# Kernel tuning notes

Measured on AMD Instinct MI355X. Metric: run time of the kernel, lower is better.

Reference implementation:

```python
import jax, jax.numpy as jnp
import numpy as np

B, S, D = 4, 1024, 1024
H = 16
DK = D // H  # per-head dim_q = dim_k = 64
DFF = 4096
EPS = 1e-5


def _layer_norm(x, g, b):
    m = jnp.mean(x, axis=-1, keepdims=True)
    v = jnp.mean((x - m) ** 2, axis=-1, keepdims=True)
    return (x - m) / jnp.sqrt(v + EPS) * g + b


def setup_inputs() -> dict:
    key = jax.random.key(0)
    ks = jax.random.split(key, 16)
    sd = 1.0 / np.sqrt(D)
    sk = 1.0 / np.sqrt(H * DK)
    sf = 1.0 / np.sqrt(DFF)
    return {
        "src": jax.random.normal(ks[0], (B, S, D), jnp.float32),
        # stacked per-head projections (torch loops over H separate nn.Linear)
        "Wq": jax.random.uniform(ks[1], (H, D, DK), jnp.float32, -sd, sd),
        "bq": jax.random.uniform(ks[2], (H, DK), jnp.float32, -sd, sd),
        "Wk": jax.random.uniform(ks[3], (H, D, DK), jnp.float32, -sd, sd),
        "bk": jax.random.uniform(ks[4], (H, DK), jnp.float32, -sd, sd),
        "Wv": jax.random.uniform(ks[5], (H, D, DK), jnp.float32, -sd, sd),
        "bv": jax.random.uniform(ks[6], (H, DK), jnp.float32, -sd, sd),
        "Wo": jax.random.uniform(ks[7], (H * DK, D), jnp.float32, -sk, sk),
        "bo": jax.random.uniform(ks[8], (D,), jnp.float32, -sk, sk),
        "g1": jnp.ones((D,), jnp.float32),
        "be1": jnp.zeros((D,), jnp.float32),
        "W1": jax.random.uniform(ks[9], (D, DFF), jnp.float32, -sd, sd),
        "b1": jax.random.uniform(ks[10], (DFF,), jnp.float32, -sd, sd),
        "W2": jax.random.uniform(ks[11], (DFF, D), jnp.float32, -sf, sf),
        "b2": jax.random.uniform(ks[12], (D,), jnp.float32, -sf, sf),
        "g2": jnp.ones((D,), jnp.float32),
        "be2": jnp.zeros((D,), jnp.float32),
    }


def reference(src, Wq, bq, Wk, bk, Wv, bv, Wo, bo, g1, be1, W1, b1, W2, b2, g2, be2):
    # multi-head attention (all heads batched via einsum instead of python loop)
    q = jnp.einsum("bsd,hdk->bhsk", src, Wq) + bq[None, :, None, :]
    k = jnp.einsum("bsd,hdk->bhsk", src, Wk) + bk[None, :, None, :]
    v = jnp.einsum("bsd,hdk->bhsk", src, Wv) + bv[None, :, None, :]
    scale = jnp.asarray(DK, src.dtype) ** 0.5  # query.size(-1) ** 0.5
    scores = jnp.einsum("bhsk,bhtk->bhst", q, k) / scale
    attn = jax.nn.softmax(scores, axis=-1)
    o = jnp.einsum("bhst,bhtk->bhsk", attn, v)  # [B,H,S,DK]
    o = o.transpose(0, 2, 1, 3).reshape(src.shape[0], src.shape[1], H * DK)
    attn_out = o @ Wo + bo
    x = _layer_norm(src + attn_out, g1, be1)
    ffn = jax.nn.relu(x @ W1 + b1) @ W2 + b2
    return _layer_norm(x + ffn, g2, be2)
```

## Files before the change

### kernel.cpp

```cpp
#include <hip/hip_runtime.h>
#include <hip/hip_bf16.h>

#define DEV __device__ __forceinline__

typedef __attribute__((ext_vector_type(8))) short bf16x8;
typedef __attribute__((ext_vector_type(4))) float f32x4;
typedef __attribute__((ext_vector_type(4))) short short4v;
typedef __attribute__((ext_vector_type(2))) unsigned uint2v;

DEV short f2bf(float f) {
    union { float f; unsigned u; } x; x.f = f;
    unsigned u = x.u;
    unsigned r = (u + 0x7fffu + ((u >> 16) & 1u)) >> 16;
    return (short)r;
}

DEV float bf2f(short s) {
    union { unsigned u; float f; } x;
    x.u = ((unsigned)(unsigned short)s) << 16;
    return x.f;
}

DEV unsigned cvtpk(float a, float b) {
    unsigned r;
    asm("v_cvt_pk_bf16_f32 %0, %1, %2" : "=v"(r) : "v"(a), "v"(b));
    return r;
}

#define GLD16(g, l)                                                         \
    __builtin_amdgcn_global_load_lds(                                       \
        (const __attribute__((address_space(1))) void*)(g),                 \
        (__attribute__((address_space(3))) void*)(l), 16, 0, 0)

#define WAITV(n) asm volatile("s_waitcnt vmcnt(" #n ")" ::: "memory")
#define SBAR()   asm volatile("s_barrier" ::: "memory")
#define LGKM0()                                              \
    asm volatile("s_waitcnt lgkmcnt(0)" ::: "memory");       \
    __builtin_amdgcn_sched_barrier(0)


__global__ __launch_bounds__(256) void k_cast(const float* __restrict__ in,
                                              short* __restrict__ out, int n4) {
    int i = blockIdx.x * 256 + threadIdx.x;
    if (i >= n4) return;
    float4 v = ((const float4*)in)[i];
    short4v o;
    o[0] = f2bf(v.x); o[1] = f2bf(v.y); o[2] = f2bf(v.z); o[3] = f2bf(v.w);
    ((short4v*)out)[i] = o;
}

__global__ __launch_bounds__(256) void k_tr(const float* __restrict__ in,
                                            short* __restrict__ out,
                                            int R, int C,
                                            long in_hs, long out_hs) {
    in  += (size_t)blockIdx.z * in_hs;
    out += (size_t)blockIdx.z * out_hs;
    __shared__ short tile[64][68];
    const int t = threadIdx.x;
    const int r0 = blockIdx.y * 64, c0 = blockIdx.x * 64;
    const int lr = t >> 4, lc4 = (t & 15) * 4;
#pragma unroll
    for (int it = 0; it < 4; ++it) {
        int r = lr + it * 16;
        float4 v = *(const float4*)(in + (size_t)(r0 + r) * C + c0 + lc4);
        tile[lc4 + 0][r] = f2bf(v.x);
        tile[lc4 + 1][r] = f2bf(v.y);
        tile[lc4 + 2][r] = f2bf(v.z);
        tile[lc4 + 3][r] = f2bf(v.w);
    }
    __syncthreads();
#pragma unroll
    for (int it = 0; it < 4; ++it) {
        int c = lr + it * 16;
        short4v o;
        o[0] = tile[c][lc4 + 0];
        o[1] = tile[c][lc4 + 1];
        o[2] = tile[c][lc4 + 2];
        o[3] = tile[c][lc4 + 3];
        *(short4v*)(out + (size_t)(c0 + c) * R + r0 + lc4) = o;
    }
}

template <int MODE>
__global__ __launch_bounds__(512, 2) void k_gemm8(
    const short* __restrict__ A, const short* __restrict__ BT,
    int K, int NT,
    const float* __restrict__ f0, const float* __restrict__ f1,
    const float* __restrict__ f2,
    void* __restrict__ o0, void* __restrict__ o1, void* __restrict__ o2) {
    __shared__ short lds[2][2][2][128 * 64];
    const int t = threadIdx.x;
    const int w = t >> 6, l = t & 63;
    const int l16 = l & 15, lg = l >> 4;
    const int wm = w >> 2, wn = w & 3;
    const int bn = blockIdx.x, bm = blockIdx.y;
    const int koff = blockIdx.z * NT * 64;
    const short* Ab = A + (size_t)bm * 256 * K + koff;
    const short* Bb = BT + (size_t)bn * 256 * K + koff;
    const int srow = l >> 3;
    const int scol = ((l & 7) ^ srow) * 8;
    const int offk0 = ((0 + lg) ^ (l16 & 7)) * 8;
    const int offk1 = ((4 + lg) ^ (l16 & 7)) * 8;

    f32x4 acc[8][4] = {};

    auto stg = [&](int buf, int op, int h, int kt) {
#pragma unroll
        for (int i = 0; i < 2; ++i) {
            int row = h * 128 + w * 16 + i * 8 + srow;
            GLD16((op ? Bb : Ab) + (size_t)row * K + (size_t)kt * 64 + scol,
                  &lds[buf][op][h][(w * 16 + i * 8) * 64]);
        }
    };

    stg(0, 0, 0, 0); stg(0, 0, 1, 0);
    stg(0, 1, 0, 0); stg(0, 1, 1, 0);
    const int t1p = (NT > 1) ? 1 : 0;
    stg(1, 1, 0, t1p); stg(1, 1, 1, t1p);
    WAITV(4);
    SBAR();

    for (int kt = 0; kt < NT; ++kt) {
        const int cur = kt & 1, nxt = cur ^ 1;
        const int t1 = (kt + 1 < NT) ? kt + 1 : NT - 1;
        const int t2 = (kt + 2 < NT) ? kt + 2 : NT - 1;
        bf16x8 a0[4][2], a1[4][2], b0[2][2], b1[2][2];

#pragma unroll
        for (int m = 0; m < 4; ++m) {
            a0[m][0] = *(const bf16x8*)&lds[cur][0][wm][(m * 16 + l16) * 64 + offk0];
            a0[m][1] = *(const bf16x8*)&lds[cur][0][wm][(m * 16 + l16) * 64 + offk1];
        }
#pragma unroll
        for (int n = 0; n < 2; ++n) {
            int r = (wn & 1) * 64 + n * 16 + l16;
            b0[n][0] = *(const bf16x8*)&lds[cur][1][wn >> 1][r * 64 + offk0];
            b0[n][1] = *(const bf16x8*)&lds[cur][1][wn >> 1][r * 64 + offk1];
        }
        stg(nxt, 0, 0, t1);
        SBAR();
        LGKM0();
        __builtin_amdgcn_s_setprio(1);
#pragma unroll
        for (int m = 0; m < 4; ++m)
#pragma unroll
            for (int n = 0; n < 2; ++n) {
                acc[m][n] = __builtin_amdgcn_mfma_f32_16x16x32_bf16(a0[m][0], b0[n][0], acc[m][n], 0, 0, 0);
                acc[m][n] = __builtin_amdgcn_mfma_f32_16x16x32_bf16(a0[m][1], b0[n][1], acc[m][n], 0, 0, 0);
            }
        __builtin_amdgcn_s_setprio(0);
        SBAR();

#pragma unroll
        for (int n = 0; n < 2; ++n) {
            int r = (wn & 1) * 64 + (n + 2) * 16 + l16;
            b1[n][0] = *(const bf16x8*)&lds[cur][1][wn >> 1][r * 64 + offk0];
            b1[n][1] = *(const bf16x8*)&lds[cur][1][wn >> 1][r * 64 + offk1];
        }
        stg(nxt, 0, 1, t1);
        SBAR();
        LGKM0();
        __builtin_amdgcn_s_setprio(1);
#pragma unroll
        for (int m = 0; m < 4; ++m)
#pragma unroll
            for (int n = 0; n < 2; ++n) {
                acc[m][n + 2] = __builtin_amdgcn_mfma_f32_16x16x32_bf16(a0[m][0], b1[n][0], acc[m][n + 2], 0, 0, 0);
                acc[m][n + 2] = __builtin_amdgcn_mfma_f32_16x16x32_bf16(a0[m][1], b1[n][1], acc[m][n + 2], 0, 0, 0);
            }
        __builtin_amdgcn_s_setprio(0);
        SBAR();

#pragma unroll
        for (int m = 0; m < 4; ++m) {
            a1[m][0] = *(const bf16x8*)&lds[cur][0][wm][((m + 4) * 16 + l16) * 64 + offk0];
            a1[m][1] = *(const bf16x8*)&lds[cur][0][wm][((m + 4) * 16 + l16) * 64 + offk1];
        }
        stg(cur, 1, 0, t2);
        SBAR();
        LGKM0();
        __builtin_amdgcn_s_setprio(1);
#pragma unroll
        for (int m = 0; m < 4; ++m)
#pragma unroll
            for (int n = 0; n < 2; ++n) {
                acc[m + 4][n + 2] = __builtin_amdgcn_mfma_f32_16x16x32_bf16(a1[m][0], b1[n][0], acc[m + 4][n + 2], 0, 0, 0);
                acc[m + 4][n + 2] = __builtin_amdgcn_mfma_f32_16x16x32_bf16(a1[m][1], b1[n][1], acc[m + 4][n + 2], 0, 0, 0);
            }
        __builtin_amdgcn_s_setprio(0);
        SBAR();

        stg(cur, 1, 1, t2);
        SBAR();
        __builtin_amdgcn_s_setprio(1);
#pragma unroll
        for (int m = 0; m < 4; ++m)
#pragma unroll
            for (int n = 0; n < 2; ++n) {
                acc[m + 4][n] = __builtin_amdgcn_mfma_f32_16x16x32_bf16(a1[m][0], b0[n][0], acc[m + 4][n], 0, 0, 0);
                acc[m + 4][n] = __builtin_amdgcn_mfma_f32_16x16x32_bf16(a1[m][1], b0[n][1], acc[m + 4][n], 0, 0, 0);
            }
        __builtin_amdgcn_s_setprio(0);
        WAITV(4);
        SBAR();
    }
    WAITV(0);

    const int N = gridDim.x * 256;
#pragma unroll
    for (int m = 0; m < 8; ++m) {
        int rowbase = bm * 256 + wm * 128 + m * 16 + lg * 4;
#pragma unroll
        for (int n = 0; n < 4; ++n) {
            int col = bn * 256 + wn * 64 + n * 16 + l16;
            if constexpr (MODE == 0) {
                int p = col >> 10, c1 = col & 1023;
                int hh = c1 >> 6, dk = c1 & 63;
                const float* bias = (p == 0) ? f0 : (p == 1) ? f1 : f2;
                float bvl = bias[c1];
                float qs = (p == 0) ? 0.18033688011112042f : 1.0f;
                int b = rowbase >> 10, s = rowbase & 1023;
                if (p == 2) {
                    short4v vv;
#pragma unroll
                    for (int rr = 0; rr < 4; ++rr) vv[rr] = f2bf(acc[m][n][rr] + bvl);
                    *(short4v*)((short*)o2 + (((size_t)(b * 16 + hh) * 64 + dk) << 10) + s) = vv;
                } else {
                    short* dst = (p == 0) ? (short*)o0 : (short*)o1;
#pragma unroll
                    for (int rr = 0; rr < 4; ++rr)
                        dst[(((size_t)(b * 16 + hh) << 10) + s + rr) * 64 + dk] =
                            f2bf((acc[m][n][rr] + bvl) * qs);
                }
            } else if constexpr (MODE == 2) {
                float bvl = f0[col];
#pragma unroll
                for (int rr = 0; rr < 4; ++rr) {
                    size_t idx = (size_t)(rowbase + rr) * N + col;
                    float y = acc[m][n][rr] + bvl;
                    ((short*)o0)[idx] = f2bf(y > 0.f ? y : 0.f);
                }
            } else {
                const int Mtot = gridDim.y * 256;
                short* dst = (blockIdx.z < 3)
                    ? (short*)o0 + (size_t)blockIdx.z * Mtot * N
                    : (short*)o1;
                size_t base = (size_t)rowbase * N + col;
#pragma unroll
                for (int rr = 0; rr < 4; ++rr)
                    dst[base + (size_t)rr * N] = f2bf(acc[m][n][rr]);
            }
        }
    }
}

__global__ __launch_bounds__(512, 4) void k_attn(const short* __restrict__ Q,
                                                 const short* __restrict__ Kt,
                                                 const short* __restrict__ VT,
                                                 short* __restrict__ O) {
    __shared__ short Kl[2][64 * 64];
    __shared__ short Vl[2][64 * 64];
    __shared__ short Pl[8][16 * 64];
    const int bh = blockIdx.x;
    const int qb = blockIdx.y;
    const int t = threadIdx.x;
    const int w = t >> 6, l = t & 63;
    const int l16 = l & 15, lg = l >> 4;
    const int sw = l16 & 7;
    const int pmask = (l16 & 7) << 1;
    const int srow = l >> 3;
    const int scol = ((l & 7) ^ srow) * 8;

    const short* Qb = Q + ((size_t)bh * 1024 + qb * 128 + w * 16 + l16) * 64 + lg * 8;
    bf16x8 qf0 = *(const bf16x8*)Qb;
    bf16x8 qf1 = *(const bf16x8*)(Qb + 32);

    const short* Kbase = Kt + (size_t)bh * (1024 * 64);
    const short* Vbase = VT + (size_t)bh * (64 * 1024);

    const float THR = 11.5415603f;

    bf16x8 ones;
#pragma unroll
    for (int i = 0; i < 8; ++i) ones[i] = (short)0x3F80;

    float m = -1e30f;
    f32x4 oacc[4] = {};
    f32x4 oaccS = {};

    auto stage = [&](int buf, int t0) {
        int roww = w * 8;
        GLD16(Kbase + (size_t)(t0 + roww + srow) * 64 + scol,
              &Kl[buf][roww * 64]);
        GLD16(Vbase + (size_t)(roww + srow) * 1024 + t0 + scol,
              &Vl[buf][roww * 64]);
    };

    auto compute = [&](int cur) {
        f32x4 s[4];
#pragma unroll
        for (int n = 0; n < 4; ++n) {
            bf16x8 kf0 = *(const bf16x8*)&Kl[cur][(n * 16 + l16) * 64 + (lg ^ sw) * 8];
            bf16x8 kf1 = *(const bf16x8*)&Kl[cur][(n * 16 + l16) * 64 + ((4 + lg) ^ sw) * 8];
            f32x4 a = {0.f, 0.f, 0.f, 0.f};
            a = __builtin_amdgcn_mfma_f32_16x16x32_bf16(kf0, qf0, a, 0, 0, 0);
            a = __builtin_amdgcn_mfma_f32_16x16x32_bf16(kf1, qf1, a, 0, 0, 0);
            s[n] = a;
        }
        float m1 = fmaxf(fmaxf(s[0][0], s[0][1]), s[0][2]);
        float m2 = fmaxf(fmaxf(s[0][3], s[1][0]), s[1][1]);
        float m3 = fmaxf(fmaxf(s[1][2], s[1][3]), s[2][0]);
        float m4 = fmaxf(fmaxf(s[2][1], s[2][2]), s[2][3]);
        float m5 = fmaxf(fmaxf(s[3][0], s[3][1]), s[3][2]);
        float mx = fmaxf(fmaxf(m1, m2), m3);
        mx = fmaxf(fmaxf(m4, m5), fmaxf(mx, s[3][3]));
        mx = fmaxf(mx, __shfl_xor(mx, 16));
        mx = fmaxf(mx, __shfl_xor(mx, 32));

        if (__any(mx > m + THR)) {
            float mn = fmaxf(m, mx);
            float al = exp2f(m - mn);
            m = mn;
#pragma unroll
            for (int n = 0; n < 4; ++n)
#pragma unroll
                for (int r = 0; r < 4; ++r) s[n][r] = exp2f(s[n][r] - m);
#pragma unroll
            for (int r = 0; r < 4; ++r) {
                float alr = __shfl(al, lg * 4 + r);
                oaccS[r] *= alr;
#pragma unroll
                for (int n = 0; n < 4; ++n) oacc[n][r] *= alr;
            }
        } else {
#pragma unroll
            for (int n = 0; n < 4; ++n)
#pragma unroll
                for (int r = 0; r < 4; ++r) s[n][r] = exp2f(s[n][r] - m);
        }
#pragma unroll
        for (int n = 0; n < 4; ++n) {
            uint2v pv;
            pv[0] = cvtpk(s[n][0], s[n][1]);
            pv[1] = cvtpk(s[n][2], s[n][3]);
            int g = (n * 4 + lg) ^ pmask;
            *(uint2v*)((char*)Pl[w] + l16 * 128 + g * 8) = pv;
        }
#pragma unroll
        for (int kk = 0; kk < 2; ++kk) {
            int gp = (8 * kk + 2 * lg) ^ pmask;
            bf16x8 pa = *(const bf16x8*)((const char*)Pl[w] + l16 * 128 + gp * 8);
            oaccS = __builtin_amdgcn_mfma_f32_16x16x32_bf16(pa, ones, oaccS, 0, 0, 0);
#pragma unroll
            for (int n = 0; n < 4; ++n) {
                bf16x8 vb = *(const bf16x8*)&Vl[cur][(n * 16 + l16) * 64 +
                                                     ((kk * 4 + lg) ^ sw) * 8];
                oacc[n] = __builtin_amdgcn_mfma_f32_16x16x32_bf16(pa, vb, oacc[n],
                                                                  0, 0, 0);
            }
        }
    };

    stage(0, 0);
    for (int ti = 0; ti < 15; ++ti) {
        int cur = ti & 1;
        stage(cur ^ 1, (ti + 1) * 64);
        WAITV(2);
        SBAR();
        compute(cur);
        SBAR();
    }
    WAITV(0);
    SBAR();
    compute(1);

    const int b = bh >> 4, h = bh & 15;
#pragma unroll
    for (int r = 0; r < 4; ++r) {
        float inv = 1.f / oaccS[r];
        size_t row = (size_t)(b * 1024 + qb * 128 + w * 16 + lg * 4 + r);
#pragma unroll
        for (int n = 0; n < 4; ++n)
            O[row * 1024 + h * 64 + n * 16 + l16] = f2bf(oacc[n][r] * inv);
    }
}

__global__ __launch_bounds__(256) void k_lnwo(const short* __restrict__ p012,
                                              const short* __restrict__ p3,
                                              const float* __restrict__ bias,
                                              const float* __restrict__ resid,
                                              const float* __restrict__ g,
                                              const float* __restrict__ be,
                                              float* __restrict__ of,
                                              short* __restrict__ ob) {
    const int row = blockIdx.x, t = threadIdx.x;
    float4 x = ((const float4*)(resid + ((size_t)row << 10)))[t];
    float4 bv = ((const float4*)bias)[t];
    x.x += bv.x; x.y += bv.y; x.z += bv.z; x.w += bv.w;
#pragma unroll
    for (int kz = 0; kz < 3; ++kz) {
        short4v p = ((const short4v*)(p012 + (((size_t)kz * 4096 + row) << 10)))[t];
        x.x += bf2f(p[0]); x.y += bf2f(p[1]); x.z += bf2f(p[2]); x.w += bf2f(p[3]);
    }
    {
        short4v p = ((const short4v*)(p3 + ((size_t)row << 10)))[t];
        x.x += bf2f(p[0]); x.y += bf2f(p[1]); x.z += bf2f(p[2]); x.w += bf2f(p[3]);
    }
    float s = x.x + x.y + x.z + x.w;
    float s2 = x.x * x.x + x.y * x.y + x.z * x.z + x.w * x.w;
#pragma unroll
    for (int mm = 1; mm < 64; mm <<= 1) {
        s += __shfl_xor(s, mm);
        s2 += __shfl_xor(s2, mm);
    }
    __shared__ float red[8];
    if ((t & 63) == 0) { red[t >> 6] = s; red[4 + (t >> 6)] = s2; }
    __syncthreads();
    s = red[0] + red[1] + red[2] + red[3];
    s2 = red[4] + red[5] + red[6] + red[7];
    float mean = s * (1.f / 1024.f);
    float var = s2 * (1.f / 1024.f) - mean * mean;
    float rstd = rsqrtf(var + 1e-5f);
    int c = t * 4;
    float4 y;
    y.x = (x.x - mean) * rstd * g[c + 0] + be[c + 0];
    y.y = (x.y - mean) * rstd * g[c + 1] + be[c + 1];
    y.z = (x.z - mean) * rstd * g[c + 2] + be[c + 2];
    y.w = (x.w - mean) * rstd * g[c + 3] + be[c + 3];
    ((float4*)(of + ((size_t)row << 10)))[t] = y;
    short4v o;
    o[0] = f2bf(y.x); o[1] = f2bf(y.y); o[2] = f2bf(y.z); o[3] = f2bf(y.w);
    ((short4v*)(ob + ((size_t)row << 10)))[t] = o;
}

__global__ __launch_bounds__(256) void k_lnred(const short* __restrict__ part,
                                               const float* __restrict__ bias,
                                               const float* __restrict__ resid,
                                               const float* __restrict__ g,
                                               const float* __restrict__ be,
                                               float* __restrict__ of) {
    const int row = blockIdx.x, t = threadIdx.x;
    float4 x = ((const float4*)(resid + ((size_t)row << 10)))[t];
    float4 bv = ((const float4*)bias)[t];
    x.x += bv.x; x.y += bv.y; x.z += bv.z; x.w += bv.w;
#pragma unroll
    for (int kz = 0; kz < 4; ++kz) {
        short4v p = ((const short4v*)(part + (((size_t)kz * 4096 + row) << 10)))[t];
        x.x += bf2f(p[0]); x.y += bf2f(p[1]); x.z += bf2f(p[2]); x.w += bf2f(p[3]);
    }
    float s = x.x + x.y + x.z + x.w;
    float s2 = x.x * x.x + x.y * x.y + x.z * x.z + x.w * x.w;
#pragma unroll
    for (int mm = 1; mm < 64; mm <<= 1) {
        s += __shfl_xor(s, mm);
        s2 += __shfl_xor(s2, mm);
    }
    __shared__ float red[8];
    if ((t & 63) == 0) { red[t >> 6] = s; red[4 + (t >> 6)] = s2; }
    __syncthreads();
    s = red[0] + red[1] + red[2] + red[3];
    s2 = red[4] + red[5] + red[6] + red[7];
    float mean = s * (1.f / 1024.f);
    float var = s2 * (1.f / 1024.f) - mean * mean;
    float rstd = rsqrtf(var + 1e-5f);
    int c = t * 4;
    float4 y;
    y.x = (x.x - mean) * rstd * g[c + 0] + be[c + 0];
    y.y = (x.y - mean) * rstd * g[c + 1] + be[c + 1];
    y.z = (x.z - mean) * rstd * g[c + 2] + be[c + 2];
    y.w = (x.w - mean) * rstd * g[c + 3] + be[c + 3];
    ((float4*)(of + ((size_t)row << 10)))[t] = y;
}

extern "C" void kernel_launch(void* const* d_in, const int* in_sizes, int n_in,
                              void* d_out, int out_size, void* d_ws, size_t ws_size,
                              hipStream_t stream) {
    (void)in_sizes; (void)n_in; (void)out_size; (void)ws_size;
    const float* src = (const float*)d_in[0];
    const float* Wq  = (const float*)d_in[1];
    const float* bq  = (const float*)d_in[2];
    const float* Wk  = (const float*)d_in[3];
    const float* bk  = (const float*)d_in[4];
    const float* Wv  = (const float*)d_in[5];
    const float* bv  = (const float*)d_in[6];
    const float* Wo  = (const float*)d_in[7];
    const float* bo  = (const float*)d_in[8];
    const float* g1  = (const float*)d_in[9];
    const float* be1 = (const float*)d_in[10];
    const float* W1  = (const float*)d_in[11];
    const float* b1  = (const float*)d_in[12];
    const float* W2  = (const float*)d_in[13];
    const float* b2  = (const float*)d_in[14];
    const float* g2  = (const float*)d_in[15];
    const float* be2 = (const float*)d_in[16];

    char* ws = (char*)d_ws;
    const size_t MB = 1048576;
    short* srcbf  = (short*)(ws + 0);
    short* Qb     = (short*)(ws + 8 * MB);
    short* Kb     = (short*)(ws + 16 * MB);
    short* VTb    = (short*)(ws + 24 * MB);
    short* h1     = (short*)(ws + 0);
    short* Obuf   = srcbf;
    short* W2T    = (short*)(ws + 32 * MB);
    float* xf     = (float*)(ws + 40 * MB);
    short* WqkvT  = (short*)(ws + 56 * MB);
    short* WoT    = (short*)(ws + 62 * MB);
    short* W1T    = (short*)(ws + 64 * MB);
    short* partWo0 = (short*)(ws + 8 * MB);
    short* partWo3 = (short*)(ws + 72 * MB);
    short* xbf    = (short*)(ws + 88 * MB);
    short* part   = (short*)(ws + 56 * MB);

    k_cast<<<4096, 256, 0, stream>>>(src, srcbf, 1048576);
    k_tr<<<dim3(1, 16, 16), 256, 0, stream>>>(Wq, WqkvT,           1024, 64, 65536, 65536);
    k_tr<<<dim3(1, 16, 16), 256, 0, stream>>>(Wk, WqkvT + 1048576, 1024, 64, 65536, 65536);
    k_tr<<<dim3(1, 16, 16), 256, 0, stream>>>(Wv, WqkvT + 2097152, 1024, 64, 65536, 65536);
    k_tr<<<dim3(16, 16, 1), 256, 0, stream>>>(Wo, WoT, 1024, 1024, 0, 0);
    k_tr<<<dim3(64, 16, 1), 256, 0, stream>>>(W1, W1T, 1024, 4096, 0, 0);
    k_tr<<<dim3(16, 64, 1), 256, 0, stream>>>(W2, W2T, 4096, 1024, 0, 0);
    k_gemm8<0><<<dim3(12, 16, 1), 512, 0, stream>>>(srcbf, WqkvT, 1024, 16,
                                                    bq, bk, bv, Qb, Kb, VTb);
    k_attn<<<dim3(64, 8), 512, 0, stream>>>(Qb, Kb, VTb, Obuf);
    k_gemm8<3><<<dim3(4, 16, 4), 512, 0, stream>>>(Obuf, WoT, 1024, 4,
                                                   nullptr, nullptr, nullptr,
                                                   partWo0, partWo3, nullptr);
    k_lnwo<<<4096, 256, 0, stream>>>(partWo0, partWo3, bo, src, g1, be1, xf, xbf);
    k_gemm8<2><<<dim3(16, 16, 1), 512, 0, stream>>>(xbf, W1T, 1024, 16,
                                                    b1, nullptr, nullptr,
                                                    h1, nullptr, nullptr);
    k_gemm8<3><<<dim3(4, 16, 4), 512, 0, stream>>>(h1, W2T, 4096, 16,
                                                   nullptr, nullptr, nullptr,
                                                   part, part + 3u * 4194304u,
                                                   nullptr);
    k_lnred<<<4096, 256, 0, stream>>>(part, b2, xf, g2, be2, (float*)d_out);
}
```

Measured before the change: 214.3 us.

## Restructure GEMM main loop with fewer barriers and fuse QKV weight transposes

The GEMM k-loop now issues both A-half loads for the next tile up front, reads all B fragments at once, and runs the four MFMA quadrants back-to-back. It uses one LDS drain and barrier before staging the B tiles for step k+2, replacing the per-quadrant barriers and lgkm waits. The goal is to cut barrier and wait stalls and let MFMA work overlap more with global-to-LDS copies, at the cost of more live fragment registers. Separately, the three Wq/Wk/Wv transpose launches are merged into a single launch.

```diff
diff --git a/kernel.cpp b/kernel.cpp
--- a/kernel.cpp
+++ b/kernel.cpp
@@ -34,9 +34,7 @@
 
 #define WAITV(n) asm volatile("s_waitcnt vmcnt(" #n ")" ::: "memory")
 #define SBAR()   asm volatile("s_barrier" ::: "memory")
-#define LGKM0()                                              \
-    asm volatile("s_waitcnt lgkmcnt(0)" ::: "memory");       \
-    __builtin_amdgcn_sched_barrier(0)
+#define LGKMDRAIN() asm volatile("s_waitcnt lgkmcnt(0)" ::: "memory")
 
 
 __global__ __launch_bounds__(256) void k_cast(const float* __restrict__ in,
@@ -78,6 +76,40 @@
         o[2] = tile[c][lc4 + 2];
         o[3] = tile[c][lc4 + 3];
         *(short4v*)(out + (size_t)(c0 + c) * R + r0 + lc4) = o;
+    }
+}
+
+__global__ __launch_bounds__(256) void k_tr3(const float* __restrict__ Wq,
+                                             const float* __restrict__ Wk,
+                                             const float* __restrict__ Wv,
+                                             short* __restrict__ out) {
+    const int z = blockIdx.z;
+    const float* in = ((z < 16) ? Wq : (z < 32) ? Wk : Wv) +
+                      (size_t)(z & 15) * 65536;
+    short* o = out + (size_t)z * 65536;
+    __shared__ short tile[64][68];
+    const int t = threadIdx.x;
+    const int r0 = blockIdx.y * 64;
+    const int lr = t >> 4, lc4 = (t & 15) * 4;
+#pragma unroll
+    for (int it = 0; it < 4; ++it) {
+        int r = lr + it * 16;
+        float4 v = *(const float4*)(in + (size_t)(r0 + r) * 64 + lc4);
+        tile[lc4 + 0][r] = f2bf(v.x);
+        tile[lc4 + 1][r] = f2bf(v.y);
+        tile[lc4 + 2][r] = f2bf(v.z);
+        tile[lc4 + 3][r] = f2bf(v.w);
+    }
+    __syncthreads();
+#pragma unroll
+    for (int it = 0; it < 4; ++it) {
+        int c = lr + it * 16;
+        short4v ov;
+        ov[0] = tile[c][lc4 + 0];
+        ov[1] = tile[c][lc4 + 1];
+        ov[2] = tile[c][lc4 + 2];
+        ov[3] = tile[c][lc4 + 3];
+        *(short4v*)(o + (size_t)c * 1024 + r0 + lc4) = ov;
     }
 }
 
@@ -124,8 +156,10 @@
         const int cur = kt & 1, nxt = cur ^ 1;
         const int t1 = (kt + 1 < NT) ? kt + 1 : NT - 1;
         const int t2 = (kt + 2 < NT) ? kt + 2 : NT - 1;
+
+        stg(nxt, 0, 0, t1); stg(nxt, 0, 1, t1);
+
         bf16x8 a0[4][2], a1[4][2], b0[2][2], b1[2][2];
-
 #pragma unroll
         for (int m = 0; m < 4; ++m) {
             a0[m][0] = *(const bf16x8*)&lds[cur][0][wm][(m * 16 + l16) * 64 + offk0];
@@ -136,10 +170,10 @@
             int r = (wn & 1) * 64 + n * 16 + l16;
             b0[n][0] = *(const bf16x8*)&lds[cur][1][wn >> 1][r * 64 + offk0];
             b0[n][1] = *(const bf16x8*)&lds[cur][1][wn >> 1][r * 64 + offk1];
-        }
-        stg(nxt, 0, 0, t1);
-        SBAR();
-        LGKM0();
+            int r2 = (wn & 1) * 64 + (n + 2) * 16 + l16;
+            b1[n][0] = *(const bf16x8*)&lds[cur][1][wn >> 1][r2 * 64 + offk0];
+            b1[n][1] = *(const bf16x8*)&lds[cur][1][wn >> 1][r2 * 64 + offk1];
+        }
         __builtin_amdgcn_s_setprio(1);
 #pragma unroll
         for (int m = 0; m < 4; ++m)
@@ -147,38 +181,15 @@
             for (int n = 0; n < 2; ++n) {
                 acc[m][n] = __builtin_amdgcn_mfma_f32_16x16x32_bf16(a0[m][0], b0[n][0], acc[m][n], 0, 0, 0);
                 acc[m][n] = __builtin_amdgcn_mfma_f32_16x16x32_bf16(a0[m][1], b0[n][1], acc[m][n], 0, 0, 0);
-            }
-        __builtin_amdgcn_s_setprio(0);
-        SBAR();
-
-#pragma unroll
-        for (int n = 0; n < 2; ++n) {
-            int r = (wn & 1) * 64 + (n + 2) * 16 + l16;
-            b1[n][0] = *(const bf16x8*)&lds[cur][1][wn >> 1][r * 64 + offk0];
-            b1[n][1] = *(const bf16x8*)&lds[cur][1][wn >> 1][r * 64 + offk1];
-        }
-        stg(nxt, 0, 1, t1);
-        SBAR();
-        LGKM0();
-        __builtin_amdgcn_s_setprio(1);
-#pragma unroll
-        for (int m = 0; m < 4; ++m)
-#pragma unroll
-            for (int n = 0; n < 2; ++n) {
                 acc[m][n + 2] = __builtin_amdgcn_mfma_f32_16x16x32_bf16(a0[m][0], b1[n][0], acc[m][n + 2], 0, 0, 0);
                 acc[m][n + 2] = __builtin_amdgcn_mfma_f32_16x16x32_bf16(a0[m][1], b1[n][1], acc[m][n + 2], 0, 0, 0);
             }
         __builtin_amdgcn_s_setprio(0);
-        SBAR();
-
 #pragma unroll
         for (int m = 0; m < 4; ++m) {
             a1[m][0] = *(const bf16x8*)&lds[cur][0][wm][((m + 4) * 16 + l16) * 64 + offk0];
             a1[m][1] = *(const bf16x8*)&lds[cur][0][wm][((m + 4) * 16 + l16) * 64 + offk1];
         }
-        stg(cur, 1, 0, t2);
-        SBAR();
-        LGKM0();
         __builtin_amdgcn_s_setprio(1);
 #pragma unroll
         for (int m = 0; m < 4; ++m)
@@ -186,21 +197,14 @@
             for (int n = 0; n < 2; ++n) {
                 acc[m + 4][n + 2] = __builtin_amdgcn_mfma_f32_16x16x32_bf16(a1[m][0], b1[n][0], acc[m + 4][n + 2], 0, 0, 0);
                 acc[m + 4][n + 2] = __builtin_amdgcn_mfma_f32_16x16x32_bf16(a1[m][1], b1[n][1], acc[m + 4][n + 2], 0, 0, 0);
-            }
-        __builtin_amdgcn_s_setprio(0);
-        SBAR();
-
-        stg(cur, 1, 1, t2);
-        SBAR();
-        __builtin_amdgcn_s_setprio(1);
-#pragma unroll
-        for (int m = 0; m < 4; ++m)
-#pragma unroll
-            for (int n = 0; n < 2; ++n) {
                 acc[m + 4][n] = __builtin_amdgcn_mfma_f32_16x16x32_bf16(a1[m][0], b0[n][0], acc[m + 4][n], 0, 0, 0);
                 acc[m + 4][n] = __builtin_amdgcn_mfma_f32_16x16x32_bf16(a1[m][1], b0[n][1], acc[m + 4][n], 0, 0, 0);
             }
         __builtin_amdgcn_s_setprio(0);
+
+        LGKMDRAIN();
+        SBAR();
+        stg(cur, 1, 0, t2); stg(cur, 1, 1, t2);
         WAITV(4);
         SBAR();
     }
@@ -513,9 +517,7 @@
     short* part   = (short*)(ws + 56 * MB);
 
     k_cast<<<4096, 256, 0, stream>>>(src, srcbf, 1048576);
-    k_tr<<<dim3(1, 16, 16), 256, 0, stream>>>(Wq, WqkvT,           1024, 64, 65536, 65536);
-    k_tr<<<dim3(1, 16, 16), 256, 0, stream>>>(Wk, WqkvT + 1048576, 1024, 64, 65536, 65536);
-    k_tr<<<dim3(1, 16, 16), 256, 0, stream>>>(Wv, WqkvT + 2097152, 1024, 64, 65536, 65536);
+    k_tr3<<<dim3(1, 16, 48), 256, 0, stream>>>(Wq, Wk, Wv, WqkvT);
     k_tr<<<dim3(16, 16, 1), 256, 0, stream>>>(Wo, WoT, 1024, 1024, 0, 0);
     k_tr<<<dim3(64, 16, 1), 256, 0, stream>>>(W1, W1T, 1024, 4096, 0, 0);
     k_tr<<<dim3(16, 64, 1), 256, 0, stream>>>(W2, W2T, 4096, 1024, 0, 0);
```

Result: faster. 209.9 us (median of 2 runs) (-2.0%).
